# Kernel optimization log

Hardware: AMD Instinct MI355X
Metric: run time of the kernel (lower is better)

Reference implementation:

```python
import jax, jax.numpy as jnp
import numpy as np
from jax import lax

BN_EPS = 1e-5


def setup_inputs() -> dict:
    key = jax.random.key(0)
    ks = jax.random.split(key, 3)
    B, N, D = 96, 20, 2048
    return {
        "x": jax.random.normal(ks[0], (B, N, D), dtype=jnp.float32),
        "conv_w": jax.random.normal(ks[1], (D, 2 * D), dtype=jnp.float32) * 0.02,
        "conv_b": jax.random.normal(ks[2], (D,), dtype=jnp.float32) * 0.02,
        "bn_gamma": jnp.ones((D,), dtype=jnp.float32),
        "bn_beta": jnp.zeros((D,), dtype=jnp.float32),
        "bn_mean": jnp.zeros((D,), dtype=jnp.float32),
        "bn_var": jnp.ones((D,), dtype=jnp.float32),
        "n_neighbor": 10,
    }


def reference(x, conv_w, conv_b, bn_gamma, bn_beta, bn_mean, bn_var, n_neighbor):
    # x: [B, N, D] -> xt: [B, D, N] (channels-first point cloud of view features)
    xt = jnp.transpose(x, (0, 2, 1))
    B, D, N = xt.shape
    k = int(n_neighbor)

    # pairwise squared distances: [B, N, N]
    sq = jnp.sum(xt * xt, axis=1, keepdims=True)            # [B, 1, N]
    inner = jnp.einsum("bdn,bdm->bnm", xt, xt)              # [B, N, N]
    adj = sq + (-2.0) * inner + jnp.transpose(sq, (0, 2, 1))

    # k nearest neighbors (smallest distance) -> idx [B, N, k]
    _, nn_idx = lax.top_k(-adj, k)

    # gather neighbor features without the O(N^2) expand: [B, D, N, k]
    neighbors = jax.vmap(lambda xb, idx: xb[:, idx])(xt, nn_idx)

    center = xt[:, :, :, None]                              # [B, D, N, 1]
    edge = jnp.concatenate(
        [jnp.broadcast_to(center, (B, D, N, k)), neighbors - center], axis=1
    )                                                       # [B, 2D, N, k]

    # 1x1 conv (GEMM over channel dim) + BatchNorm (inference) + ReLU
    y = jnp.einsum("oc,bcnk->bonk", conv_w, edge) + conv_b[None, :, None, None]
    inv = bn_gamma / jnp.sqrt(bn_var + BN_EPS)
    y = y * inv[None, :, None, None] + (bn_beta - bn_mean * inv)[None, :, None, None]
    y = jax.nn.relu(y)

    # max over neighbors, then max over points -> [B, D, 1, 1]
    y = jnp.max(y, axis=-1, keepdims=True)
    y = jnp.max(y, axis=2, keepdims=True)
    return y
```

## Files before the change

kernel.cpp:

```cpp
#include <hip/hip_runtime.h>
#include <hip/hip_bf16.h>
#include <math.h>

#define BN_EPS 1e-5f
#define B_  96
#define N_  20
#define D_  2048
#define K_  10
#define M_  (B_*N_)
#define R_  (2*D_)

typedef __attribute__((ext_vector_type(8))) short bf16x8;
typedef __attribute__((ext_vector_type(4))) float f32x4;
typedef __attribute__((ext_vector_type(8))) unsigned short ushort8;

static __device__ __forceinline__ unsigned short f2bf(float f) {
  unsigned int u = __builtin_bit_cast(unsigned int, f);
  u = u + 0x7fffu + ((u >> 16) & 1u);
  return (unsigned short)(u >> 16);
}

#define GLOAD_LDS16(g, l) \
  __builtin_amdgcn_global_load_lds((const __attribute__((address_space(1))) void*)(g), \
                                   (__attribute__((address_space(3))) void*)(l), 16, 0, 0)

__global__ __launch_bounds__(512) void prep_kernel(const float* __restrict__ x,
                                                   const float* __restrict__ cw,
                                                   int* __restrict__ nn_idx,
                                                   unsigned short* __restrict__ Xb,
                                                   unsigned short* __restrict__ Wn)
{
  int t = threadIdx.x;
  if (blockIdx.x >= B_) {
    int cb = blockIdx.x - B_;
    for (int i = cb*512 + t; i < R_*D_/8; i += 416*512) {
      int r = i >> 8;
      int k = (i & 255) * 8;
      const float* src = cw + (size_t)(r >> 1) * R_ + ((r & 1) << 11) + k;
      float4 a = *(const float4*)src, c = *(const float4*)(src + 4);
      ushort8 o = { f2bf(a.x), f2bf(a.y), f2bf(a.z), f2bf(a.w),
                    f2bf(c.x), f2bf(c.y), f2bf(c.z), f2bf(c.w) };
      *((ushort8*)Wn + i) = o;
    }
    return;
  }
  int b = blockIdx.x, w = t >> 6, lane = t & 63;
  __shared__ float innr[N_*N_];
  __shared__ float adjl[N_*N_];
  const float* xb = x + (size_t)b * N_ * D_;
  int rows[3] = { w, 15 - w, (w < 4) ? 16 + w : -1 };
  #pragma unroll
  for (int ri = 0; ri < 3; ++ri) {
    int n = rows[ri];
    if (n < 0) continue;
    const float4* xnp = (const float4*)(xb + n * D_);
    float4 xn[8];
    #pragma unroll
    for (int j = 0; j < 8; ++j) xn[j] = xnp[lane + 64*j];
    for (int m = n; m < N_; ++m) {
      const float4* xmp = (const float4*)(xb + m * D_);
      float s0 = 0.f, s1 = 0.f, s2 = 0.f, s3 = 0.f;
      #pragma unroll
      for (int j = 0; j < 8; ++j) {
        float4 v = xmp[lane + 64*j];
        float d = fmaf(xn[j].x, v.x, fmaf(xn[j].y, v.y,
                  fmaf(xn[j].z, v.z, xn[j].w * v.w)));
        if      ((j&3)==0) s0 += d;
        else if ((j&3)==1) s1 += d;
        else if ((j&3)==2) s2 += d;
        else               s3 += d;
      }
      float s = (s0 + s1) + (s2 + s3);
      #pragma unroll
      for (int off = 32; off > 0; off >>= 1)
        s += __shfl_xor(s, off, 64);
      if (lane == 0) { innr[n*N_+m] = s; innr[m*N_+n] = s; }
    }
  }
  __syncthreads();
  for (int p = t; p < N_*N_; p += 512) {
    int n = p / N_, m = p % N_;
    adjl[p] = innr[n*N_+n] + innr[m*N_+m] - 2.f * innr[p];
  }
  __syncthreads();
  if (t < N_) {
    int n = t;
    unsigned mask = 0;
    for (int it = 0; it < K_; ++it) {
      float bv = INFINITY; int bi = 0;
      for (int m = 0; m < N_; ++m) {
        if (!((mask >> m) & 1u)) {
          float v = adjl[n*N_+m];
          if (v < bv) { bv = v; bi = m; }
        }
      }
      mask |= 1u << bi;
      nn_idx[(b*N_ + n)*K_ + it] = bi;
    }
  }
  unsigned short* xo = Xb + (size_t)b * N_ * D_;
  for (int i = t; i < N_*D_/8; i += 512) {
    const float4* src = (const float4*)xb + (size_t)i * 2;
    float4 a = src[0], c = src[1];
    ushort8 o = { f2bf(a.x), f2bf(a.y), f2bf(a.z), f2bf(a.w),
                  f2bf(c.x), f2bf(c.y), f2bf(c.z), f2bf(c.w) };
    *((ushort8*)xo + i) = o;
  }
}

__global__ __launch_bounds__(256, 4) void fused_gemm(
    const unsigned short* __restrict__ Xb, const unsigned short* __restrict__ Wn,
    const int* __restrict__ nn_idx, const float* __restrict__ conv_b,
    const float* __restrict__ gamma, const float* __restrict__ beta,
    const float* __restrict__ mean, const float* __restrict__ var,
    float* __restrict__ out)
{
  __shared__ __align__(16) char smem[44160];
  unsigned short* As = (unsigned short*)smem;
  unsigned short* Bs = (unsigned short*)(smem + 10240);
  float* Cl  = (float*)smem;
  int*   idxl = (int*)(smem + 40960);

  int flat = blockIdx.y * 24 + blockIdx.x;
  int nf = (flat & 7) * 96 + (flat >> 3);
  int bx = nf % 24, by = nf / 24;

  int t = threadIdx.x, lane = t & 63, w = t >> 6;
  int m0 = bx * 80, b0 = bx * 4;
  int r0 = by * 128, o0 = by * 64;
  int rowsel = lane & 15, ksel = lane >> 4;

  for (int i = t; i < 4*N_*K_; i += 256) idxl[i] = nn_idx[b0*N_*K_ + i];

  f32x4 acc[5][2] = {};

  for (int k0 = 0; k0 < D_; k0 += 64) {
    #pragma unroll
    for (int i = 0; i < 3; ++i) {
      int fl = i*256 + t;
      if (fl < 640) {
        int row = fl >> 3, kc = fl & 7;
        GLOAD_LDS16(Xb + (size_t)(m0 + row) * D_ + k0 + ((kc ^ (row & 7)) << 3),
                    As + fl*8);
      }
    }
    #pragma unroll
    for (int i = 0; i < 4; ++i) {
      int fl = i*256 + t;
      int row = fl >> 3, kc = fl & 7;
      GLOAD_LDS16(Wn + (size_t)(r0 + row) * D_ + k0 + ((kc ^ (row & 7)) << 3),
                  Bs + fl*8);
    }
    __syncthreads();
    #pragma unroll
    for (int ks = 0; ks < 2; ++ks) {
      int swz = ((ks*4 + ksel) ^ (rowsel & 7)) << 3;
      bf16x8 a[5], bfr[2];
      #pragma unroll
      for (int mi = 0; mi < 5; ++mi)
        a[mi] = *(const bf16x8*)(As + (mi*16 + rowsel)*64 + swz);
      #pragma unroll
      for (int ri = 0; ri < 2; ++ri)
        bfr[ri] = *(const bf16x8*)(Bs + (w*32 + ri*16 + rowsel)*64 + swz);
      #pragma unroll
      for (int mi = 0; mi < 5; ++mi)
        #pragma unroll
        for (int ri = 0; ri < 2; ++ri)
          acc[mi][ri] = __builtin_amdgcn_mfma_f32_16x16x32_bf16(a[mi], bfr[ri], acc[mi][ri], 0, 0, 0);
    }
    __syncthreads();
  }

  #pragma unroll
  for (int mi = 0; mi < 5; ++mi)
    #pragma unroll
    for (int ri = 0; ri < 2; ++ri)
      #pragma unroll
      for (int rg = 0; rg < 4; ++rg)
        Cl[(mi*16 + ksel*4 + rg)*128 + w*32 + ri*16 + rowsel] = acc[mi][ri][rg];
  __syncthreads();

  int bb = w, oo = lane;
  int og = o0 + oo;
  float invv  = gamma[og] / sqrtf(var[og] + BN_EPS);
  float shift = fmaf(-mean[og], invv, beta[og]);
  float bias  = conv_b[og];
  float best = 0.f;
  int rbase = bb * N_;
  for (int n = 0; n < N_; ++n) {
    float Pv = Cl[(rbase + n)*128 + oo*2];
    float Qn = Cl[(rbase + n)*128 + oo*2 + 1];
    float aa = Pv - Qn + bias;
    const int* ix = idxl + bb*N_*K_ + n*K_;
    #pragma unroll
    for (int kk = 0; kk < K_; ++kk) {
      int j = ix[kk];
      float v = fmaf(aa + Cl[(rbase + j)*128 + oo*2 + 1], invv, shift);
      best = fmaxf(best, v);
    }
  }
  out[(size_t)(b0 + bb) * D_ + og] = best;
}

extern "C" void kernel_launch(void* const* d_in, const int* in_sizes, int n_in,
                              void* d_out, int out_size, void* d_ws, size_t ws_size,
                              hipStream_t stream)
{
  const float* x      = (const float*)d_in[0];
  const float* conv_w = (const float*)d_in[1];
  const float* conv_b = (const float*)d_in[2];
  const float* gamma  = (const float*)d_in[3];
  const float* beta   = (const float*)d_in[4];
  const float* mean   = (const float*)d_in[5];
  const float* var    = (const float*)d_in[6];

  int* nn_idx = (int*)d_ws;
  unsigned short* Xb = (unsigned short*)((char*)d_ws + 76800);
  unsigned short* Wn = (unsigned short*)((char*)d_ws + 76800 + (size_t)M_*D_*2);

  prep_kernel<<<B_ + 416, 512, 0, stream>>>(x, conv_w, nn_idx, Xb, Wn);
  fused_gemm<<<dim3(24, 32), 256, 0, stream>>>(
      Xb, Wn, nn_idx, conv_b, gamma, beta, mean, var, (float*)d_out);
}
```

Measured before the change: 77.46 us.

## Double-buffer GEMM LDS tiles, fuse Gram row loops, widen weight conversion grid

The GEMM main loop now keeps two LDS stages, so the async global-to-LDS loads for the next K tile are issued before the MFMAs on the current tile run. This halves the barriers per iteration, but the larger LDS footprint means the occupancy hint drops from 4 to 2 blocks. The prep kernel computes all three Gram rows owned by a wave in one pass over m, reading each x row once instead of up to three times. It also launches more blocks for the weight-to-bf16 conversion.

```diff
diff --git a/kernel.cpp b/kernel.cpp
--- a/kernel.cpp
+++ b/kernel.cpp
@@ -33,7 +33,7 @@
   int t = threadIdx.x;
   if (blockIdx.x >= B_) {
     int cb = blockIdx.x - B_;
-    for (int i = cb*512 + t; i < R_*D_/8; i += 416*512) {
+    for (int i = cb*512 + t; i < R_*D_/8; i += 928*512) {
       int r = i >> 8;
       int k = (i & 255) * 8;
       const float* src = cw + (size_t)(r >> 1) * R_ + ((r & 1) << 11) + k;
@@ -48,33 +48,39 @@
   __shared__ float innr[N_*N_];
   __shared__ float adjl[N_*N_];
   const float* xb = x + (size_t)b * N_ * D_;
-  int rows[3] = { w, 15 - w, (w < 4) ? 16 + w : -1 };
+  int n1 = w, n2 = 15 - w, n3 = (w < 4) ? 16 + w : -1;
+  float4 c1[8], c2[8], c3[8];
+  const float4* p1 = (const float4*)(xb + n1 * D_);
+  const float4* p2 = (const float4*)(xb + n2 * D_);
   #pragma unroll
-  for (int ri = 0; ri < 3; ++ri) {
-    int n = rows[ri];
-    if (n < 0) continue;
-    const float4* xnp = (const float4*)(xb + n * D_);
-    float4 xn[8];
-    #pragma unroll
-    for (int j = 0; j < 8; ++j) xn[j] = xnp[lane + 64*j];
-    for (int m = n; m < N_; ++m) {
-      const float4* xmp = (const float4*)(xb + m * D_);
-      float s0 = 0.f, s1 = 0.f, s2 = 0.f, s3 = 0.f;
-      #pragma unroll
-      for (int j = 0; j < 8; ++j) {
-        float4 v = xmp[lane + 64*j];
-        float d = fmaf(xn[j].x, v.x, fmaf(xn[j].y, v.y,
-                  fmaf(xn[j].z, v.z, xn[j].w * v.w)));
-        if      ((j&3)==0) s0 += d;
-        else if ((j&3)==1) s1 += d;
-        else if ((j&3)==2) s2 += d;
-        else               s3 += d;
-      }
-      float s = (s0 + s1) + (s2 + s3);
-      #pragma unroll
-      for (int off = 32; off > 0; off >>= 1)
-        s += __shfl_xor(s, off, 64);
-      if (lane == 0) { innr[n*N_+m] = s; innr[m*N_+n] = s; }
+  for (int j = 0; j < 8; ++j) { c1[j] = p1[lane + 64*j]; c2[j] = p2[lane + 64*j]; }
+  if (n3 >= 0) {
+    const float4* p3 = (const float4*)(xb + n3 * D_);
+    #pragma unroll
+    for (int j = 0; j < 8; ++j) c3[j] = p3[lane + 64*j];
+  }
+  for (int m = 0; m < N_; ++m) {
+    bool d1 = (m >= n1), d2 = (m >= n2), d3 = (n3 >= 0) && (m >= n3);
+    if (!(d1 | d2 | d3)) continue;
+    const float4* pm = (const float4*)(xb + m * D_);
+    float s1 = 0.f, s2 = 0.f, s3 = 0.f;
+    #pragma unroll
+    for (int j = 0; j < 8; ++j) {
+      float4 v = pm[lane + 64*j];
+      if (d1) s1 = fmaf(c1[j].x, v.x, fmaf(c1[j].y, v.y, fmaf(c1[j].z, v.z, fmaf(c1[j].w, v.w, s1))));
+      if (d2) s2 = fmaf(c2[j].x, v.x, fmaf(c2[j].y, v.y, fmaf(c2[j].z, v.z, fmaf(c2[j].w, v.w, s2))));
+      if (d3) s3 = fmaf(c3[j].x, v.x, fmaf(c3[j].y, v.y, fmaf(c3[j].z, v.z, fmaf(c3[j].w, v.w, s3))));
+    }
+    #pragma unroll
+    for (int off = 32; off > 0; off >>= 1) {
+      s1 += __shfl_xor(s1, off, 64);
+      s2 += __shfl_xor(s2, off, 64);
+      s3 += __shfl_xor(s3, off, 64);
+    }
+    if (lane == 0) {
+      if (d1) { innr[n1*N_+m] = s1; innr[m*N_+n1] = s1; }
+      if (d2) { innr[n2*N_+m] = s2; innr[m*N_+n2] = s2; }
+      if (d3) { innr[n3*N_+m] = s3; innr[m*N_+n3] = s3; }
     }
   }
   __syncthreads();
@@ -108,18 +114,16 @@
   }
 }
 
-__global__ __launch_bounds__(256, 4) void fused_gemm(
+__global__ __launch_bounds__(256, 2) void fused_gemm(
     const unsigned short* __restrict__ Xb, const unsigned short* __restrict__ Wn,
     const int* __restrict__ nn_idx, const float* __restrict__ conv_b,
     const float* __restrict__ gamma, const float* __restrict__ beta,
     const float* __restrict__ mean, const float* __restrict__ var,
     float* __restrict__ out)
 {
-  __shared__ __align__(16) char smem[44160];
-  unsigned short* As = (unsigned short*)smem;
-  unsigned short* Bs = (unsigned short*)(smem + 10240);
+  __shared__ __align__(16) char smem[56448];
   float* Cl  = (float*)smem;
-  int*   idxl = (int*)(smem + 40960);
+  int*   idxl = (int*)(smem + 53248);
 
   int flat = blockIdx.y * 24 + blockIdx.x;
   int nf = (flat & 7) * 96 + (flat >> 3);
@@ -134,14 +138,16 @@
 
   f32x4 acc[5][2] = {};
 
-  for (int k0 = 0; k0 < D_; k0 += 64) {
+  auto stage = [&](int sel, int k0) {
+    unsigned short* Asb = (unsigned short*)(smem + sel*26624);
+    unsigned short* Bsb = (unsigned short*)(smem + sel*26624 + 10240);
     #pragma unroll
     for (int i = 0; i < 3; ++i) {
       int fl = i*256 + t;
       if (fl < 640) {
         int row = fl >> 3, kc = fl & 7;
         GLOAD_LDS16(Xb + (size_t)(m0 + row) * D_ + k0 + ((kc ^ (row & 7)) << 3),
-                    As + fl*8);
+                    Asb + fl*8);
       }
     }
     #pragma unroll
@@ -149,27 +155,38 @@
       int fl = i*256 + t;
       int row = fl >> 3, kc = fl & 7;
       GLOAD_LDS16(Wn + (size_t)(r0 + row) * D_ + k0 + ((kc ^ (row & 7)) << 3),
-                  Bs + fl*8);
-    }
-    __syncthreads();
+                  Bsb + fl*8);
+    }
+  };
+
+  auto compute = [&](int sel) {
+    unsigned short* Asb = (unsigned short*)(smem + sel*26624);
+    unsigned short* Bsb = (unsigned short*)(smem + sel*26624 + 10240);
     #pragma unroll
     for (int ks = 0; ks < 2; ++ks) {
       int swz = ((ks*4 + ksel) ^ (rowsel & 7)) << 3;
       bf16x8 a[5], bfr[2];
       #pragma unroll
       for (int mi = 0; mi < 5; ++mi)
-        a[mi] = *(const bf16x8*)(As + (mi*16 + rowsel)*64 + swz);
+        a[mi] = *(const bf16x8*)(Asb + (mi*16 + rowsel)*64 + swz);
       #pragma unroll
       for (int ri = 0; ri < 2; ++ri)
-        bfr[ri] = *(const bf16x8*)(Bs + (w*32 + ri*16 + rowsel)*64 + swz);
+        bfr[ri] = *(const bf16x8*)(Bsb + (w*32 + ri*16 + rowsel)*64 + swz);
       #pragma unroll
       for (int mi = 0; mi < 5; ++mi)
         #pragma unroll
         for (int ri = 0; ri < 2; ++ri)
           acc[mi][ri] = __builtin_amdgcn_mfma_f32_16x16x32_bf16(a[mi], bfr[ri], acc[mi][ri], 0, 0, 0);
     }
+  };
+
+  stage(0, 0);
+  for (int kt = 0; kt < D_/64; ++kt) {
     __syncthreads();
-  }
+    if (kt + 1 < D_/64) stage((kt+1) & 1, (kt+1)*64);
+    compute(kt & 1);
+  }
+  __syncthreads();
 
   #pragma unroll
   for (int mi = 0; mi < 5; ++mi)
@@ -218,7 +235,7 @@
   unsigned short* Xb = (unsigned short*)((char*)d_ws + 76800);
   unsigned short* Wn = (unsigned short*)((char*)d_ws + 76800 + (size_t)M_*D_*2);
 
-  prep_kernel<<<B_ + 416, 512, 0, stream>>>(x, conv_w, nn_idx, Xb, Wn);
+  prep_kernel<<<1024, 512, 0, stream>>>(x, conv_w, nn_idx, Xb, Wn);
   fused_gemm<<<dim3(24, 32), 256, 0, stream>>>(
       Xb, Wn, nn_idx, conv_b, gamma, beta, mean, var, (float*)d_out);
 }
```

Result: slower. 114.1 us (+47.3%).
